# Kernel tuning notes

Measured on AMD Instinct MI355X. Metric: run time of the kernel, lower is better.

The kernel has to match this reference:

```python
import jax, jax.numpy as jnp
import numpy as np

NEG_INF = -1e30

def setup_inputs() -> dict:
    key = jax.random.key(0)
    ks = jax.random.split(key, 7)
    B, S, D = 2, 4096, 128
    scale = 1.0 / np.sqrt(D)
    return {
        "x": jax.random.normal(ks[0], (B, S, D), jnp.float32),
        "Wq": jax.random.normal(ks[1], (D, D), jnp.float32) * scale,
        "bq": jax.random.normal(ks[2], (D,), jnp.float32) * 0.01,
        "Wk": jax.random.normal(ks[3], (D, D), jnp.float32) * scale,
        "bk": jax.random.normal(ks[4], (D,), jnp.float32) * 0.01,
        "Wv": jax.random.normal(ks[5], (D, D), jnp.float32) * scale,
        "bv": jax.random.normal(ks[6], (D,), jnp.float32) * 0.01,
        "window_size": 128,
    }

def reference(x, Wq, bq, Wk, bk, Wv, bv, window_size):
    B, S, D = x.shape
    half = window_size // 2
    q = x @ Wq + bq
    k = x @ Wk + bk
    v = x @ Wv + bv
    # banded window indices: for query i, keys in [i-half, i+half]
    offs = jnp.arange(-half, half + 1)          # [W] with W = 2*half+1
    idx = jnp.arange(S)[:, None] + offs[None, :]  # [S, W]
    valid = (idx >= 0) & (idx < S)
    idxc = jnp.clip(idx, 0, S - 1)
    kw = k[:, idxc, :]  # [B, S, W, D]
    vw = v[:, idxc, :]  # [B, S, W, D]
    scores = jnp.einsum('bsd,bswd->bsw', q, kw) / jnp.sqrt(jnp.float32(D))
    scores = jnp.where(valid[None], scores, NEG_INF)
    attn = jax.nn.softmax(scores, axis=-1)
    out = jnp.einsum('bsw,bswd->bsd', attn, vw)
    return out
```

## Files before the change

kernel.cpp:

```cpp
#include <hip/hip_runtime.h>
#include <hip/hip_bf16.h>

typedef __attribute__((ext_vector_type(8))) short short8;
typedef __attribute__((ext_vector_type(4))) float f32x4;

union U16x8 { uint4 u; short8 s; unsigned short us[8]; };

#define S_LEN 4096
#define DH    128
#define TQ    16
#define KEYS  160
#define VTS   168
#define PST   168

__global__ __launch_bounds__(256) void qkv_kernel(
    const float* __restrict__ x,
    const float* __restrict__ Wq, const float* __restrict__ bq,
    const float* __restrict__ Wk, const float* __restrict__ bk,
    const float* __restrict__ Wv, const float* __restrict__ bv,
    __hip_bfloat16* __restrict__ q, __hip_bfloat16* __restrict__ k,
    __hip_bfloat16* __restrict__ v)
{
    const int t = threadIdx.x;
    const int j = t & 127;
    const int g = t >> 7;
    const int row0 = blockIdx.x * 16;

    __shared__ float xs[16][DH];
    for (int c = t; c < 512; c += 256) {
        int r = c >> 5, f = c & 31;
        ((float4*)xs[r])[f] = ((const float4*)(x + (size_t)(row0 + r) * DH))[f];
    }
    __syncthreads();

    float aq[8], ak[8], av[8];
    const float bqv = bq[j], bkv = bk[j], bvv = bv[j];
    #pragma unroll
    for (int r = 0; r < 8; ++r) { aq[r] = bqv; ak[r] = bkv; av[r] = bvv; }

    #pragma unroll 2
    for (int d4 = 0; d4 < 32; ++d4) {
        float4 xv[8];
        #pragma unroll
        for (int r = 0; r < 8; ++r) xv[r] = *(const float4*)&xs[g*8 + r][d4*4];
        #pragma unroll
        for (int dd = 0; dd < 4; ++dd) {
            int d = d4*4 + dd;
            float wq = Wq[d*DH + j], wk = Wk[d*DH + j], wv = Wv[d*DH + j];
            #pragma unroll
            for (int r = 0; r < 8; ++r) {
                float xvs = (&xv[r].x)[dd];
                aq[r] = fmaf(xvs, wq, aq[r]);
                ak[r] = fmaf(xvs, wk, ak[r]);
                av[r] = fmaf(xvs, wv, av[r]);
            }
        }
    }
    #pragma unroll
    for (int r = 0; r < 8; ++r) {
        size_t o = (size_t)(row0 + g*8 + r) * DH + j;
        q[o] = __float2bfloat16(aq[r]);
        k[o] = __float2bfloat16(ak[r]);
        v[o] = __float2bfloat16(av[r]);
    }
}

__device__ inline void vt_xpose_write(unsigned short* VT, const uint4* vr,
                                      int kgp, int dgp)
{
    unsigned w[8][4];
    #pragma unroll
    for (int p = 0; p < 4; ++p) {
        #pragma unroll
        for (int j = 0; j < 4; ++j) {
            unsigned xlo = ((const unsigned*)&vr[2*p])[j];
            unsigned ylo = ((const unsigned*)&vr[2*p+1])[j];
            w[2*j][p]   = __builtin_amdgcn_perm(ylo, xlo, 0x05040100u);
            w[2*j+1][p] = __builtin_amdgcn_perm(ylo, xlo, 0x07060302u);
        }
    }
    int sw = kgp + (dgp & 7); if (sw >= 21) sw -= 21;
    #pragma unroll
    for (int d = 0; d < 8; ++d) {
        int row = dgp*8 + d;
        *(uint4*)&VT[row*VTS + sw*8] =
            make_uint4(w[d][0], w[d][1], w[d][2], w[d][3]);
    }
}

__global__ __launch_bounds__(256) void attn_kernel(
    const __hip_bfloat16* __restrict__ qg,
    const __hip_bfloat16* __restrict__ kg,
    const __hip_bfloat16* __restrict__ vg,
    float* __restrict__ out, const int* __restrict__ wsz)
{
    __shared__ __align__(16) unsigned short VT[128 * VTS];
    __shared__ __align__(16) unsigned short Pm[TQ * PST];
    __shared__ float pmax[4][16];
    __shared__ float psum[4][16];

    const int t    = threadIdx.x;
    const int wave = t >> 6, lane = t & 63;
    const int i = lane & 15, g = lane >> 4;
    const int qblk = blockIdx.x;
    const int b    = qblk >> 8;
    const int s0   = (qblk & 255) * TQ;
    const int k0   = s0 - 64;
    const int half = wsz[0] >> 1;
    const float scale = 0.08838834764831845f;

    const __hip_bfloat16* kb = kg + (size_t)b * S_LEN * DH;
    const __hip_bfloat16* vb = vg + (size_t)b * S_LEN * DH;

    const int kgp0 = t >> 4, dgp0 = t & 15;
    const bool two = (t & 3) == 0;
    const int tau2 = 256 + (t >> 2);
    const int kgp1 = tau2 >> 4, dgp1 = tau2 & 15;
    uint4 vr0[8], vr1[8];
    #pragma unroll
    for (int r = 0; r < 8; ++r) {
        int key = k0 + kgp0*8 + r;
        uint4 val = make_uint4(0u,0u,0u,0u);
        if (key >= 0 && key < S_LEN)
            val = *(const uint4*)(vb + (size_t)key * DH + dgp0*8);
        vr0[r] = val;
    }
    #pragma unroll
    for (int r = 0; r < 8; ++r) {
        int key = k0 + kgp1*8 + r;
        uint4 val = make_uint4(0u,0u,0u,0u);
        if (two && key >= 0 && key < S_LEN)
            val = *(const uint4*)(vb + (size_t)key * DH + dgp1*8);
        vr1[r] = val;
    }

    short8 aq[4];
    {
        const __hip_bfloat16* qrow = qg + (size_t)(b * S_LEN + s0 + i) * DH;
        #pragma unroll
        for (int kc = 0; kc < 4; ++kc) {
            U16x8 u; u.u = *(const uint4*)(qrow + kc*32 + g*8);
            aq[kc] = u.s;
        }
    }

    const int nkt = (wave < 2) ? 3 : 2;
    f32x4 acc[3];
    #pragma unroll
    for (int u = 0; u < 3; ++u) { acc[u][0]=0.f; acc[u][1]=0.f; acc[u][2]=0.f; acc[u][3]=0.f; }
    #pragma unroll
    for (int u = 0; u < 3; ++u) {
        if (u < nkt) {
            int kt = wave + 4*u;
            int key = k0 + kt*16 + i;
            const __hip_bfloat16* krow = kb + (ptrdiff_t)key * DH;
            #pragma unroll
            for (int kc = 0; kc < 4; ++kc) {
                U16x8 u16v; u16v.u = *(const uint4*)(krow + kc*32 + g*8);
                acc[u] = __builtin_amdgcn_mfma_f32_16x16x32_bf16(aq[kc], u16v.s, acc[u], 0, 0, 0);
            }
        }
    }

    vt_xpose_write(VT, vr0, kgp0, dgp0);
    if (two) vt_xpose_write(VT, vr1, kgp1, dgp1);

    float sc[3][4], m4[4];
    #pragma unroll
    for (int r = 0; r < 4; ++r) m4[r] = -3e30f;
    #pragma unroll
    for (int u = 0; u < 3; ++u) {
        if (u < nkt) {
            int kt = wave + 4*u;
            int key = k0 + kt*16 + i;
            #pragma unroll
            for (int r = 0; r < 4; ++r) {
                int qrow = s0 + g*4 + r;
                bool valid = (key >= 0) && (key < S_LEN) &&
                             (key >= qrow - half) && (key <= qrow + half);
                float sv = valid ? acc[u][r] * scale : -1e30f;
                sc[u][r] = sv;
                m4[r] = fmaxf(m4[r], sv);
            }
        }
    }
    #pragma unroll
    for (int r = 0; r < 4; ++r) {
        #pragma unroll
        for (int m = 1; m < 16; m <<= 1)
            m4[r] = fmaxf(m4[r], __shfl_xor(m4[r], m, 64));
    }
    if (i == 0) {
        #pragma unroll
        for (int r = 0; r < 4; ++r) pmax[wave][g*4 + r] = m4[r];
    }
    __syncthreads();

    float M[4], l4[4];
    #pragma unroll
    for (int r = 0; r < 4; ++r) {
        int qr = g*4 + r;
        M[r] = fmaxf(fmaxf(pmax[0][qr], pmax[1][qr]), fmaxf(pmax[2][qr], pmax[3][qr]));
        l4[r] = 0.f;
    }
    #pragma unroll
    for (int u = 0; u < 3; ++u) {
        if (u < nkt) {
            int kt = wave + 4*u;
            #pragma unroll
            for (int r = 0; r < 4; ++r) {
                float p = __expf(sc[u][r] - M[r]);
                l4[r] += p;
                __hip_bfloat16 pb = __float2bfloat16(p);
                Pm[(g*4 + r) * PST + kt*16 + i] = *(unsigned short*)&pb;
            }
        }
    }
    #pragma unroll
    for (int r = 0; r < 4; ++r) {
        #pragma unroll
        for (int m = 1; m < 16; m <<= 1)
            l4[r] += __shfl_xor(l4[r], m, 64);
    }
    if (i == 0) {
        #pragma unroll
        for (int r = 0; r < 4; ++r) psum[wave][g*4 + r] = l4[r];
    }
    __syncthreads();

    float linv[4];
    #pragma unroll
    for (int r = 0; r < 4; ++r) {
        int qr = g*4 + r;
        linv[r] = 1.0f / (psum[0][qr] + psum[1][qr] + psum[2][qr] + psum[3][qr]);
    }

    short8 ap[5];
    #pragma unroll
    for (int kc = 0; kc < 5; ++kc)
        ap[kc] = *(const short8*)&Pm[i * PST + kc*32 + g*8];

    const int n0 = wave * 32;
    f32x4 oacc[2];
    #pragma unroll
    for (int nt = 0; nt < 2; ++nt) { oacc[nt][0]=0.f; oacc[nt][1]=0.f; oacc[nt][2]=0.f; oacc[nt][3]=0.f; }
    #pragma unroll
    for (int nt = 0; nt < 2; ++nt) {
        int row0 = n0 + nt*16 + i;
        int dgr = (row0 >> 3) & 7;
        #pragma unroll
        for (int kc = 0; kc < 5; ++kc) {
            int lg = 4*kc + g;
            int sw = lg + dgr; if (sw >= 21) sw -= 21;
            short8 bv = *(const short8*)&VT[row0 * VTS + sw*8];
            oacc[nt] = __builtin_amdgcn_mfma_f32_16x16x32_bf16(ap[kc], bv, oacc[nt], 0, 0, 0);
        }
    }

    #pragma unroll
    for (int nt = 0; nt < 2; ++nt) {
        #pragma unroll
        for (int r = 0; r < 4; ++r) {
            int qrow = s0 + g*4 + r;
            out[((size_t)(b * S_LEN) + qrow) * DH + n0 + nt*16 + i] = oacc[nt][r] * linv[r];
        }
    }
}

extern "C" void kernel_launch(void* const* d_in, const int* in_sizes, int n_in,
                              void* d_out, int out_size, void* d_ws, size_t ws_size,
                              hipStream_t stream) {
    const float* x  = (const float*)d_in[0];
    const float* Wq = (const float*)d_in[1];
    const float* bq = (const float*)d_in[2];
    const float* Wk = (const float*)d_in[3];
    const float* bk = (const float*)d_in[4];
    const float* Wv = (const float*)d_in[5];
    const float* bv = (const float*)d_in[6];
    const int* wsz  = (const int*)d_in[7];

    const int B = 2, S = 4096;
    const int N = B * S;

    __hip_bfloat16* q = (__hip_bfloat16*)d_ws;
    __hip_bfloat16* k = q + (size_t)N * DH;
    __hip_bfloat16* v = k + (size_t)N * DH;

    qkv_kernel<<<N / 16, 256, 0, stream>>>(x, Wq, bq, Wk, bk, Wv, bv, q, k, v);
    attn_kernel<<<N / TQ, 256, 0, stream>>>(q, k, v, (float*)d_out, wsz);
}
```

Baseline: 99.84 us.

## Compute QKV projection with bf16 MFMA using hi/lo split of x

Replaces the scalar fp32 FMA QKV projection with MFMA 16x16x32 bf16 instructions. Each block now covers 32 rows. x is split into high and low bf16 parts to keep accuracy, while the weights are rounded to bf16 and read with strided global loads. The aim is to cut the ALU cost of the projection stage, at the price of weight precision and uncoalesced weight loads.

```diff
diff --git a/kernel.cpp b/kernel.cpp
--- a/kernel.cpp
+++ b/kernel.cpp
@@ -9,9 +9,9 @@
 #define S_LEN 4096
 #define DH    128
 #define TQ    16
-#define KEYS  160
 #define VTS   168
 #define PST   168
+#define XSTR  136
 
 __global__ __launch_bounds__(256) void qkv_kernel(
     const float* __restrict__ x,
@@ -21,47 +21,89 @@
     __hip_bfloat16* __restrict__ q, __hip_bfloat16* __restrict__ k,
     __hip_bfloat16* __restrict__ v)
 {
+    __shared__ __align__(16) unsigned short XH[32 * XSTR];
+    __shared__ __align__(16) unsigned short XL[32 * XSTR];
+
     const int t = threadIdx.x;
-    const int j = t & 127;
-    const int g = t >> 7;
-    const int row0 = blockIdx.x * 16;
-
-    __shared__ float xs[16][DH];
-    for (int c = t; c < 512; c += 256) {
-        int r = c >> 5, f = c & 31;
-        ((float4*)xs[r])[f] = ((const float4*)(x + (size_t)(row0 + r) * DH))[f];
+    const int row0 = blockIdx.x * 32;
+
+    #pragma unroll
+    for (int p = 0; p < 4; ++p) {
+        int c = t + p * 256;
+        int r = c >> 5, cg = c & 31;
+        float4 xv = *(const float4*)(x + (size_t)(row0 + r) * DH + cg * 4);
+        unsigned h[2], l[2];
+        #pragma unroll
+        for (int hw = 0; hw < 2; ++hw) {
+            unsigned hh[2], ll[2];
+            #pragma unroll
+            for (int j = 0; j < 2; ++j) {
+                float xs = (&xv.x)[hw * 2 + j];
+                __hip_bfloat16 hb = __float2bfloat16(xs);
+                float hf = __bfloat162float(hb);
+                __hip_bfloat16 lb = __float2bfloat16(xs - hf);
+                hh[j] = *(unsigned short*)&hb;
+                ll[j] = *(unsigned short*)&lb;
+            }
+            h[hw] = hh[0] | (hh[1] << 16);
+            l[hw] = ll[0] | (ll[1] << 16);
+        }
+        *(uint2*)&XH[r * XSTR + cg * 4] = make_uint2(h[0], h[1]);
+        *(uint2*)&XL[r * XSTR + cg * 4] = make_uint2(l[0], l[1]);
     }
     __syncthreads();
 
-    float aq[8], ak[8], av[8];
-    const float bqv = bq[j], bkv = bk[j], bvv = bv[j];
-    #pragma unroll
-    for (int r = 0; r < 8; ++r) { aq[r] = bqv; ak[r] = bkv; av[r] = bvv; }
-
-    #pragma unroll 2
-    for (int d4 = 0; d4 < 32; ++d4) {
-        float4 xv[8];
-        #pragma unroll
-        for (int r = 0; r < 8; ++r) xv[r] = *(const float4*)&xs[g*8 + r][d4*4];
-        #pragma unroll
-        for (int dd = 0; dd < 4; ++dd) {
-            int d = d4*4 + dd;
-            float wq = Wq[d*DH + j], wk = Wk[d*DH + j], wv = Wv[d*DH + j];
-            #pragma unroll
-            for (int r = 0; r < 8; ++r) {
-                float xvs = (&xv[r].x)[dd];
-                aq[r] = fmaf(xvs, wq, aq[r]);
-                ak[r] = fmaf(xvs, wk, ak[r]);
-                av[r] = fmaf(xvs, wv, av[r]);
-            }
-        }
-    }
-    #pragma unroll
-    for (int r = 0; r < 8; ++r) {
-        size_t o = (size_t)(row0 + g*8 + r) * DH + j;
-        q[o] = __float2bfloat16(aq[r]);
-        k[o] = __float2bfloat16(ak[r]);
-        v[o] = __float2bfloat16(av[r]);
+    const int wave = t >> 6, lane = t & 63;
+    const int i = lane & 15, g = lane >> 4;
+
+    short8 ah[2][4], al[2][4];
+    #pragma unroll
+    for (int rt = 0; rt < 2; ++rt)
+        #pragma unroll
+        for (int kc = 0; kc < 4; ++kc) {
+            ah[rt][kc] = *(const short8*)&XH[(rt*16 + i) * XSTR + kc*32 + g*8];
+            al[rt][kc] = *(const short8*)&XL[(rt*16 + i) * XSTR + kc*32 + g*8];
+        }
+
+    const float* Ws[3] = {Wq, Wk, Wv};
+    const float* Bs[3] = {bq, bk, bv};
+    __hip_bfloat16* Os[3] = {q, k, v};
+
+    #pragma unroll
+    for (int mat = 0; mat < 3; ++mat) {
+        #pragma unroll
+        for (int ct = 0; ct < 2; ++ct) {
+            const int col = wave*32 + ct*16 + i;
+            const float bias = Bs[mat][col];
+
+            short8 bf[4];
+            #pragma unroll
+            for (int kc = 0; kc < 4; ++kc) {
+                const float* wp = Ws[mat] + (size_t)(kc*32 + g*8) * DH + col;
+                U16x8 u;
+                #pragma unroll
+                for (int j = 0; j < 8; ++j) {
+                    __hip_bfloat16 wb = __float2bfloat16(wp[(size_t)j * DH]);
+                    u.us[j] = *(unsigned short*)&wb;
+                }
+                bf[kc] = u.s;
+            }
+
+            #pragma unroll
+            for (int rt = 0; rt < 2; ++rt) {
+                f32x4 acc; acc[0]=0.f; acc[1]=0.f; acc[2]=0.f; acc[3]=0.f;
+                #pragma unroll
+                for (int kc = 0; kc < 4; ++kc) {
+                    acc = __builtin_amdgcn_mfma_f32_16x16x32_bf16(ah[rt][kc], bf[kc], acc, 0, 0, 0);
+                    acc = __builtin_amdgcn_mfma_f32_16x16x32_bf16(al[rt][kc], bf[kc], acc, 0, 0, 0);
+                }
+                #pragma unroll
+                for (int r = 0; r < 4; ++r) {
+                    Os[mat][(size_t)(row0 + rt*16 + g*4 + r) * DH + col] =
+                        __float2bfloat16(acc[r] + bias);
+                }
+            }
+        }
     }
 }
 
@@ -286,6 +328,6 @@
     __hip_bfloat16* k = q + (size_t)N * DH;
     __hip_bfloat16* v = k + (size_t)N * DH;
 
-    qkv_kernel<<<N / 16, 256, 0, stream>>>(x, Wq, bq, Wk, bk, Wv, bv, q, k, v);
+    qkv_kernel<<<N / 32, 256, 0, stream>>>(x, Wq, bq, Wk, bk, Wv, bv, q, k, v);
     attn_kernel<<<N / TQ, 256, 0, stream>>>(q, k, v, (float*)d_out, wsz);
 }
```

Result: faster. 95.73 us (-4.1%).
